# Kernel tuning notes

Hardware: AMD Instinct MI355X
Metric: run time of the kernel (lower is better)

The kernel has to match this reference:

```python
import jax, jax.numpy as jnp
import numpy as np

# Module config (mirrors PlateYoloBlock __init__)
IMAGE_W, IMAGE_H = 2048, 2048
GRID_SIZE = 8
GRID_W = IMAGE_W // GRID_SIZE  # 256
GRID_H = IMAGE_H // GRID_SIZE  # 256
BBOX_ATTRS = 13


def _xy_offset():
    # np.meshgrid(arange(grid_w), arange(grid_h)) stacked on axis=2 -> (grid_h, grid_w, 2)
    # [..., 0] = x (column) index, [..., 1] = y (row) index
    gx = jnp.arange(GRID_W, dtype=jnp.float32)
    gy = jnp.arange(GRID_H, dtype=jnp.float32)
    xx, yy = jnp.meshgrid(gx, gy)  # each (grid_h, grid_w)
    return jnp.stack([xx, yy], axis=-1)  # (grid_h, grid_w, 2)


def setup_inputs() -> dict:
    key = jax.random.key(0)
    coordinates = jax.random.normal(key, (32, BBOX_ATTRS, GRID_H, GRID_W), dtype=jnp.float32)
    return {"coordinates": coordinates}


def reference(coordinates) -> jnp.ndarray:
    # Inference path of PlateYoloBlock.forward (target=None):
    #   permute (B,13,H,W) -> (B,H,W,13)
    #   xy   = sigmoid(raw[..., :2]) + grid offset
    #   wh   = exp(raw[..., 2:4])
    #   conf = sigmoid(raw[..., -1])
    #   all-but-conf scaled by grid_size; reshape to (B, grid_w*grid_h, 13)
    b = coordinates.shape[0]
    c = jnp.transpose(coordinates, (0, 2, 3, 1))  # (B, grid_h, grid_w, 13)
    xy = jax.nn.sigmoid(c[..., :2]) + _xy_offset()[None]  # (B,H,W,2)
    wh = jnp.exp(c[..., 2:4])
    corners = c[..., 4:12]  # raw 4-corner coords, untouched by activations
    conf = jax.nn.sigmoid(c[..., 12:13])
    boxes = jnp.concatenate([xy, wh, corners], axis=-1) * jnp.float32(GRID_SIZE)
    out = jnp.concatenate([boxes, conf], axis=-1)  # (B,H,W,13)
    return out.reshape(b, GRID_W * GRID_H, BBOX_ATTRS)
```

## Files before the change

kernel.cpp:

```cpp
#include <hip/hip_runtime.h>


#define NB      32
#define NC      13
#define HW      65536
#define WIDTH   256
#define THREADS 256
#define PPT     4
#define TILE    (THREADS * PPT)
#define NBLOCKS ((NB * HW) / TILE)

typedef float v4f __attribute__((ext_vector_type(4)));

__device__ __forceinline__ float sigmoidf_(float x) {
    return 1.0f / (1.0f + __expf(-x));
}

__global__ __launch_bounds__(THREADS) void plate_yolo_kernel(
        const float* __restrict__ in, float* __restrict__ out) {
    const int tid = threadIdx.x;
    const long long s0 = (long long)blockIdx.x * TILE;
    const int b = (int)(s0 >> 16);
    const int posBase = (int)(s0 & (HW - 1));
    const float* __restrict__ inB = in + (long long)b * NC * HW + posBase;

    const int p0   = tid * PPT;
    const int pos0 = posBase + p0;
    const float fx0 = (float)(pos0 & (WIDTH - 1));
    const float fy  = (float)(pos0 >> 8);

    v4f v[NC];
    #pragma unroll
    for (int c = 0; c < NC; ++c) {
        v[c] = *(const v4f*)(inB + c * HW + p0);
    }

    float res[PPT * NC];
    #pragma unroll
    for (int c = 0; c < NC; ++c) {
        #pragma unroll
        for (int q = 0; q < PPT; ++q) {
            const float x = v[c][q];
            float r;
            if (c == 0)                 r = (sigmoidf_(x) + (fx0 + (float)q)) * 8.0f;
            else if (c == 1)            r = (sigmoidf_(x) + fy) * 8.0f;
            else if (c == 2 || c == 3)  r = __expf(x) * 8.0f;
            else if (c == 12)           r = sigmoidf_(x);
            else                        r = x * 8.0f;
            res[q * NC + c] = r;
        }
    }

    v4f* __restrict__ dst = (v4f*)(out + (s0 + p0) * NC);
    #pragma unroll
    for (int j = 0; j < NC; ++j) {
        v4f w;
        w[0] = res[4*j + 0]; w[1] = res[4*j + 1];
        w[2] = res[4*j + 2]; w[3] = res[4*j + 3];
        dst[j] = w;
    }
}

extern "C" void kernel_launch(void* const* d_in, const int* in_sizes, int n_in,
                              void* d_out, int out_size, void* d_ws, size_t ws_size,
                              hipStream_t stream) {
    const float* in = (const float*)d_in[0];
    float* out = (float*)d_out;
    plate_yolo_kernel<<<NBLOCKS, THREADS, 0, stream>>>(in, out);
}
```

Measured before the change: 218.4 us.

## Stage transpose through LDS with double-buffered register prefetch over sub-tiles

Each block now handles several 512-position sub-tiles. For each sub-tile it loads channel-major vectors, computes the activations, scatters the results into LDS in position-major layout, and then writes fully contiguous coalesced float4 stores. Register double-buffering prefetches the next sub-tile's loads while the current one is computed. The goal is to replace the strided per-thread 52-byte output stores with coalesced writes and to overlap load latency with work. In exchange the kernel adds LDS bank conflicts on the stride-13 scatter, two barriers per sub-tile, higher register use, and fewer blocks.

```diff
diff --git a/kernel.cpp b/kernel.cpp
--- a/kernel.cpp
+++ b/kernel.cpp
@@ -6,9 +6,11 @@
 #define HW      65536
 #define WIDTH   256
 #define THREADS 256
-#define PPT     4
-#define TILE    (THREADS * PPT)
+#define SUB     512
+#define NT      4
+#define TILE    (SUB * NT)
 #define NBLOCKS ((NB * HW) / TILE)
+#define NSLOT   (SUB * NC / 4)
 
 typedef float v4f __attribute__((ext_vector_type(4)));
 
@@ -18,46 +20,80 @@
 
 __global__ __launch_bounds__(THREADS) void plate_yolo_kernel(
         const float* __restrict__ in, float* __restrict__ out) {
+    __shared__ float lds[SUB * NC];
+
     const int tid = threadIdx.x;
     const long long s0 = (long long)blockIdx.x * TILE;
     const int b = (int)(s0 >> 16);
     const int posBase = (int)(s0 & (HW - 1));
     const float* __restrict__ inB = in + (long long)b * NC * HW + posBase;
 
-    const int p0   = tid * PPT;
-    const int pos0 = posBase + p0;
-    const float fx0 = (float)(pos0 & (WIDTH - 1));
-    const float fy  = (float)(pos0 >> 8);
+    v4f vA[7], vB[7];
 
-    v4f v[NC];
+    auto load_tile = [&](int t, v4f* dst) {
+        const float* base = inB + t * SUB;
+        #pragma unroll
+        for (int k = 0; k < 7; ++k) {
+            const int s = tid + k * THREADS;
+            if (s < NSLOT)
+                dst[k] = *(const v4f*)(base + (s >> 7) * HW + ((s & 127) << 2));
+        }
+    };
+
+    load_tile(0, vA);
+
     #pragma unroll
-    for (int c = 0; c < NC; ++c) {
-        v[c] = *(const v4f*)(inB + c * HW + p0);
-    }
+    for (int t = 0; t < NT; ++t) {
+        v4f* cur = (t & 1) ? vB : vA;
+        v4f* nxt = (t & 1) ? vA : vB;
 
-    float res[PPT * NC];
-    #pragma unroll
-    for (int c = 0; c < NC; ++c) {
+        if (t + 1 < NT) load_tile(t + 1, nxt);
+        __builtin_amdgcn_sched_barrier(0);
+
         #pragma unroll
-        for (int q = 0; q < PPT; ++q) {
-            const float x = v[c][q];
-            float r;
-            if (c == 0)                 r = (sigmoidf_(x) + (fx0 + (float)q)) * 8.0f;
-            else if (c == 1)            r = (sigmoidf_(x) + fy) * 8.0f;
-            else if (c == 2 || c == 3)  r = __expf(x) * 8.0f;
-            else if (c == 12)           r = sigmoidf_(x);
-            else                        r = x * 8.0f;
-            res[q * NC + c] = r;
+        for (int k = 0; k < 7; ++k) {
+            const int s = tid + k * THREADS;
+            if (s < NSLOT) {
+                const int c  = s >> 7;
+                const int pl = (s & 127) << 2;
+                #pragma unroll
+                for (int q = 0; q < 4; ++q) {
+                    const float x = cur[k][q];
+                    const int p = pl + q;
+                    float r;
+                    if (c == 0) {
+                        const int pos = posBase + t * SUB + p;
+                        r = (sigmoidf_(x) + (float)(pos & (WIDTH - 1))) * 8.0f;
+                    } else if (c == 1) {
+                        const int pos = posBase + t * SUB + p;
+                        r = (sigmoidf_(x) + (float)(pos >> 8)) * 8.0f;
+                    } else if (c == 2 || c == 3) {
+                        r = __expf(x) * 8.0f;
+                    } else if (c == 12) {
+                        r = sigmoidf_(x);
+                    } else {
+                        r = x * 8.0f;
+                    }
+                    lds[p * NC + c] = r;
+                }
+            }
         }
-    }
 
-    v4f* __restrict__ dst = (v4f*)(out + (s0 + p0) * NC);
-    #pragma unroll
-    for (int j = 0; j < NC; ++j) {
-        v4f w;
-        w[0] = res[4*j + 0]; w[1] = res[4*j + 1];
-        w[2] = res[4*j + 2]; w[3] = res[4*j + 3];
-        dst[j] = w;
+        asm volatile("s_waitcnt lgkmcnt(0)" ::: "memory");
+        __builtin_amdgcn_s_barrier();
+
+        {
+            const v4f* __restrict__ src4 = (const v4f*)lds;
+            v4f* __restrict__ dst4 = (v4f*)(out + (s0 + t * SUB) * NC);
+            #pragma unroll
+            for (int k = 0; k < 7; ++k) {
+                const int s = tid + k * THREADS;
+                if (s < NSLOT) dst4[s] = src4[s];
+            }
+        }
+
+        asm volatile("s_waitcnt lgkmcnt(0)" ::: "memory");
+        __builtin_amdgcn_s_barrier();
     }
 }
 
```

New measurement: 193.7 us. 1.13x faster.
